# Kernel tuning notes

Measured on AMD Instinct MI355X. Metric: run time of the kernel, lower is better.

Reference implementation:

```python
import jax, jax.numpy as jnp
import numpy as np

HEAD_DIM = 128
PROJ_DIM = 64


def setup_inputs() -> dict:
    key = jax.random.key(0)
    kq, kk, kv, kr = jax.random.split(key, 4)
    B, H, NQ, NKV = 1, 16, 2048, 4096
    Q = jax.random.normal(kq, (B, H, NQ, HEAD_DIM), dtype=jnp.float32)
    K = jax.random.normal(kk, (B, H, NKV, HEAD_DIM), dtype=jnp.float32)
    V = jax.random.normal(kv, (B, H, NKV, HEAD_DIM), dtype=jnp.float32)
    # R ~ N(0,1) / sqrt(proj_dim), as in the torch __init__
    R = jax.random.normal(kr, (HEAD_DIM, PROJ_DIM), dtype=jnp.float32) / (PROJ_DIM ** 0.5)
    return {"Q": Q, "K": K, "V": V, "R": R}


def reference(Q, K, V, R):
    proj_dim = R.shape[-1]
    scale = 1.0 / (proj_dim ** 0.5)
    # Project Q and K into the random-projection space: [B,H,N,proj_dim]
    Q_proj = jnp.einsum('bhnd,dp->bhnp', Q, R)
    K_proj = jnp.einsum('bhmd,dp->bhmp', K, R)
    # scores: [B,H,NQ,NKV]
    scores = jnp.einsum('bhnp,bhmp->bhnm', Q_proj, K_proj) * scale
    weights = jax.nn.softmax(scores, axis=-1)
    # output: [B,H,NQ,head_dim]
    return jnp.einsum('bhnm,bhmd->bhnd', weights, V)
```

## Files before the change

### kernel.cpp

```cpp
#include <hip/hip_runtime.h>

#define HEADS 16
#define NQ    2048
#define NKV   4096
#define DH    128
#define PDIM  64

typedef __bf16 bf16_t;
typedef bf16_t bf16x8 __attribute__((ext_vector_type(8)));
typedef bf16_t bf16x4 __attribute__((ext_vector_type(4)));
typedef bf16_t bf16x2 __attribute__((ext_vector_type(2)));
typedef float  f32x4  __attribute__((ext_vector_type(4)));
typedef float  f32x16 __attribute__((ext_vector_type(16)));
typedef int    i32x4  __attribute__((ext_vector_type(4)));

typedef __attribute__((address_space(3))) unsigned int       lds_u32;
typedef __attribute__((address_space(1))) const unsigned int glb_u32;

__device__ __forceinline__ void dma16(const void* g, void* l) {
  __builtin_amdgcn_global_load_lds((glb_u32*)g, (lds_u32*)l, 16, 0, 0);
}

__global__ __launch_bounds__(256) void rprep_kernel(
    const float* __restrict__ R, bf16_t* __restrict__ Rbt)
{
  const int tid = threadIdx.x;
#pragma unroll
  for (int rep = 0; rep < 32; ++rep) {
    const int idx = tid + rep * 256;
    const int n = idx & 63, k = idx >> 6;
    Rbt[n * 128 + k] = (bf16_t)R[k * 64 + n];
  }
}

__global__ __launch_bounds__(256) void proj_kernel(
    const float* __restrict__ Q, const float* __restrict__ K,
    const bf16_t* __restrict__ Rbt,
    bf16_t* __restrict__ Qp, bf16_t* __restrict__ Kp)
{
  __shared__ bf16_t sY[4][16 * 72];
  const int tid = threadIdx.x;
  const int bid = blockIdx.x;

  const int isQ = (bid < 512);
  const float* src = isQ ? Q : K;
  const long row0  = isQ ? (long)bid * 64 : (long)(bid - 512) * 64;
  const float scale = isQ ? 0.18033688011112042f : 1.0f;
  bf16_t* Y = isQ ? Qp : Kp;

  const int wave = tid >> 6, lane = tid & 63;
  const int n16  = lane & 15, quad = lane >> 4;

  bf16x8 bfr[4][4];
#pragma unroll
  for (int nt = 0; nt < 4; ++nt)
#pragma unroll
    for (int kk = 0; kk < 4; ++kk)
      bfr[nt][kk] = *(const bf16x8*)(Rbt + (nt * 16 + n16) * 128 + kk * 32 + quad * 8);

  const int arow = wave * 16 + n16;
  const float* xp = src + (row0 + arow) * DH;
  bf16x8 a[4];
#pragma unroll
  for (int kk = 0; kk < 4; ++kk) {
    const int k0 = kk * 32 + quad * 8;
    f32x4 x0 = *(const f32x4*)(xp + k0);
    f32x4 x1 = *(const f32x4*)(xp + k0 + 4);
    bf16x8 av;
#pragma unroll
    for (int j = 0; j < 4; ++j) { av[j] = (bf16_t)(x0[j] * scale); av[4 + j] = (bf16_t)(x1[j] * scale); }
    a[kk] = av;
  }

  bf16_t* sy = sY[wave];
#pragma unroll
  for (int nt = 0; nt < 4; ++nt) {
    f32x4 acc = {0.f, 0.f, 0.f, 0.f};
#pragma unroll
    for (int kk = 0; kk < 4; ++kk)
      acc = __builtin_amdgcn_mfma_f32_16x16x32_bf16(a[kk], bfr[nt][kk], acc, 0, 0, 0);
#pragma unroll
    for (int r = 0; r < 4; ++r)
      sy[(quad * 4 + r) * 72 + nt * 16 + n16] = (bf16_t)acc[r];
  }
  const long xrow = row0 + wave * 16;
  const int row = lane >> 2, cg = lane & 3;
  bf16x8 w0 = *(const bf16x8*)(&sy[row * 72 + cg * 16]);
  bf16x8 w1 = *(const bf16x8*)(&sy[row * 72 + cg * 16 + 8]);
  *(bf16x8*)(Y + (xrow + row) * PDIM + cg * 16)     = w0;
  *(bf16x8*)(Y + (xrow + row) * PDIM + cg * 16 + 8) = w1;
}

__global__ __launch_bounds__(256) void vtrans_kernel(
    const float* __restrict__ V, bf16_t* __restrict__ Vt)
{
  __shared__ float sF[64 * 128];
  const int tid = threadIdx.x;
  const int bid = blockIdx.x;

  const float* tp = V + (long)bid * 64 * DH;
#pragma unroll
  for (int rep = 0; rep < 8; ++rep) {
    const int slot = tid + rep * 256;
    const int j = slot >> 5, g = slot & 31;
    f32x4 v = *(const f32x4*)(tp + j * DH + g * 4);
    *(f32x4*)(&sF[j * 128 + ((g ^ ((j >> 3) & 7)) << 2)]) = v;
  }
  __syncthreads();

  const int h = bid >> 6, jt = bid & 63;
  bf16_t* op = Vt + (long)h * DH * NKV + jt * 64;
#pragma unroll
  for (int rep = 0; rep < 4; ++rep) {
    const int slot = tid + rep * 256;
    const int d = slot >> 3, j8 = (slot & 7) * 8;
    const int key = slot & 7;
    const int gsw = (((d >> 2) ^ key) << 2) + (d & 3);
    bf16x8 w;
#pragma unroll
    for (int jj = 0; jj < 8; ++jj) w[jj] = (bf16_t)sF[(j8 + jj) * 128 + gsw];
    *(bf16x8*)(op + (long)d * NKV + j8) = w;
  }
}

__global__ __launch_bounds__(128, 2) void flash_kernel(
    const bf16_t* __restrict__ Qp, const bf16_t* __restrict__ Kp,
    const bf16_t* __restrict__ Vt, bf16_t* __restrict__ Opart,
    float* __restrict__ Lpart, float* __restrict__ Out,
    int splits, int iters)
{
  __shared__ char smem[24576];
  bf16_t* sK = (bf16_t*)smem;
  bf16_t* sV = (bf16_t*)(smem + 8192);

  const int tid  = threadIdx.x;
  const int wave = tid >> 6, lane = tid & 63;
  const int l31  = lane & 31, h = lane >> 5;

  const int head = blockIdx.x & 15;
  const int qt   = (blockIdx.x >> 4) & 15;
  const int sp   = blockIdx.x >> 8;

  const int qbase = qt * 128 + wave * 64;
  const int kv0   = sp * (64 * iters);

  bf16x8 qf[2][4];
#pragma unroll
  for (int qsub = 0; qsub < 2; ++qsub)
#pragma unroll
    for (int k = 0; k < 4; ++k)
      qf[qsub][k] = *(const bf16x8*)(Qp + ((long)head * NQ + qbase + qsub * 32 + l31) * PDIM
                                     + k * 16 + h * 8);

  f32x16 o[2][4] = {};
  float rsum[2] = {0.f, 0.f};

  const bf16_t* kpH = Kp + (long)head * NKV * PDIM;
  const bf16_t* vtH = Vt + (long)head * DH * NKV;

  const int sw = ((lane & 7) ^ ((lane >> 3) & 7)) * 8;
  const int r8 = lane >> 3;

  for (int t = 0; t < iters; ++t) {
    const int kvb = kv0 + t * 64;
    __syncthreads();
    if (wave == 0) {
#pragma unroll
      for (int i = 0; i < 8; ++i)
        dma16(kpH + (long)(kvb + i * 8 + r8) * PDIM + sw, smem + i * 1024);
#pragma unroll
      for (int i = 0; i < 4; ++i)
        dma16(vtH + (long)(i * 8 + r8) * NKV + kvb + sw, smem + 8192 + i * 1024);
    } else {
#pragma unroll
      for (int i = 4; i < 16; ++i)
        dma16(vtH + (long)(i * 8 + r8) * NKV + kvb + sw, smem + 8192 + i * 1024);
    }
    __syncthreads();

#pragma unroll
    for (int s = 0; s < 2; ++s) {
      int bfr[2][2][4];
#pragma unroll
      for (int qsub = 0; qsub < 2; ++qsub) {
        f32x16 sc = {};
        const int r = s * 32 + l31;
#pragma unroll
        for (int k = 0; k < 4; ++k) {
          const int c = 2 * k + h;
          const bf16x8 a = *(const bf16x8*)(sK + r * 64 + ((c ^ (r & 7)) * 8));
          sc = __builtin_amdgcn_mfma_f32_32x32x16_bf16(a, qf[qsub][k], sc, 0, 0, 0);
        }
        int pk[4][2];
#pragma unroll
        for (int rg = 0; rg < 4; ++rg) {
          const float p0 = __builtin_amdgcn_exp2f(sc[rg * 4 + 0]);
          const float p1 = __builtin_amdgcn_exp2f(sc[rg * 4 + 1]);
          const float p2 = __builtin_amdgcn_exp2f(sc[rg * 4 + 2]);
          const float p3 = __builtin_amdgcn_exp2f(sc[rg * 4 + 3]);
          rsum[qsub] += (p0 + p1) + (p2 + p3);
          union { bf16x2 v; int i; } u0, u1;
          u0.v = bf16x2{(bf16_t)p0, (bf16_t)p1};
          u1.v = bf16x2{(bf16_t)p2, (bf16_t)p3};
          pk[rg][0] = u0.i; pk[rg][1] = u1.i;
        }
#pragma unroll
        for (int cl = 0; cl < 2; ++cl) {
          const int e00 = __shfl_xor(pk[2 * cl][0], 32);
          const int e01 = __shfl_xor(pk[2 * cl][1], 32);
          const int e10 = __shfl_xor(pk[2 * cl + 1][0], 32);
          const int e11 = __shfl_xor(pk[2 * cl + 1][1], 32);
          bfr[qsub][cl][0] = h ? e10 : pk[2 * cl][0];
          bfr[qsub][cl][1] = h ? e11 : pk[2 * cl][1];
          bfr[qsub][cl][2] = h ? pk[2 * cl + 1][0] : e00;
          bfr[qsub][cl][3] = h ? pk[2 * cl + 1][1] : e01;
        }
      }
#pragma unroll
      for (int dsub = 0; dsub < 4; ++dsub) {
        const int r = dsub * 32 + l31;
#pragma unroll
        for (int cl = 0; cl < 2; ++cl) {
          const int c = 2 * (2 * s + cl) + h;
          const bf16x8 va = *(const bf16x8*)(sV + r * 64 + ((c ^ (r & 7)) * 8));
#pragma unroll
          for (int qsub = 0; qsub < 2; ++qsub) {
            union { i32x4 i; bf16x8 v; } pb;
            pb.i = i32x4{bfr[qsub][cl][0], bfr[qsub][cl][1],
                         bfr[qsub][cl][2], bfr[qsub][cl][3]};
            o[qsub][dsub] = __builtin_amdgcn_mfma_f32_32x32x16_bf16(va, pb.v, o[qsub][dsub], 0, 0, 0);
          }
        }
      }
    }
  }

  __syncthreads();
  bf16_t* myT = (bf16_t*)(smem + wave * 8704);
#pragma unroll
  for (int qsub = 0; qsub < 2; ++qsub) {
    const float lsum = rsum[qsub] + __shfl_xor(rsum[qsub], 32);
    const float scale = (splits > 1) ? 1.0f : (1.0f / lsum);
#pragma unroll
    for (int dsub = 0; dsub < 4; ++dsub)
#pragma unroll
      for (int rg = 0; rg < 4; ++rg) {
        bf16x4 w = { (bf16_t)(o[qsub][dsub][rg * 4 + 0] * scale),
                     (bf16_t)(o[qsub][dsub][rg * 4 + 1] * scale),
                     (bf16_t)(o[qsub][dsub][rg * 4 + 2] * scale),
                     (bf16_t)(o[qsub][dsub][rg * 4 + 3] * scale) };
        *(bf16x4*)(myT + l31 * 136 + dsub * 32 + rg * 8 + h * 4) = w;
      }
    const int qglob = qbase + qsub * 32;
#pragma unroll
    for (int j = 0; j < 8; ++j) {
      const int ql = j * 4 + (lane >> 4);
      bf16x8 v = *(const bf16x8*)(myT + ql * 136 + (lane & 15) * 8);
      if (splits > 1) {
        *(bf16x8*)(Opart + (((long)sp * HEADS + head) * NQ + qglob + ql) * DH + (lane & 15) * 8) = v;
      } else {
        float* op = Out + ((long)head * NQ + qglob + ql) * DH + (lane & 15) * 8;
        f32x4 a = {(float)v[0], (float)v[1], (float)v[2], (float)v[3]};
        f32x4 b = {(float)v[4], (float)v[5], (float)v[6], (float)v[7]};
        *(f32x4*)op = a; *(f32x4*)(op + 4) = b;
      }
    }
    if (splits > 1 && h == 0)
      Lpart[((long)sp * HEADS + head) * NQ + qglob + l31] = lsum;
  }
}

__global__ __launch_bounds__(256) void combine_kernel(
    const bf16_t* __restrict__ Opart, const float* __restrict__ Lpart,
    float* __restrict__ Out)
{
  const long idx = (long)blockIdx.x * 256 + threadIdx.x;
  const int  d8  = (int)(idx & 15);
  const long hq  = idx >> 4;
  float l = 0.f;
  float acc[8];
#pragma unroll
  for (int j = 0; j < 8; ++j) acc[j] = 0.f;
#pragma unroll
  for (int s = 0; s < 4; ++s) {
    l += Lpart[s * (long)(HEADS * NQ) + hq];
    bf16x8 v = *(const bf16x8*)(Opart + (s * (long)(HEADS * NQ) + hq) * DH + d8 * 8);
#pragma unroll
    for (int j = 0; j < 8; ++j) acc[j] += (float)v[j];
  }
  const float inv = 1.f / l;
  f32x4 o0 = { acc[0] * inv, acc[1] * inv, acc[2] * inv, acc[3] * inv };
  f32x4 o1 = { acc[4] * inv, acc[5] * inv, acc[6] * inv, acc[7] * inv };
  float* op = Out + hq * DH + d8 * 8;
  *(f32x4*)(op)     = o0;
  *(f32x4*)(op + 4) = o1;
}

extern "C" void kernel_launch(void* const* d_in, const int* in_sizes, int n_in,
                              void* d_out, int out_size, void* d_ws, size_t ws_size,
                              hipStream_t stream)
{
  const float* Q = (const float*)d_in[0];
  const float* K = (const float*)d_in[1];
  const float* V = (const float*)d_in[2];
  const float* R = (const float*)d_in[3];
  float* Out = (float*)d_out;

  char* ws = (char*)d_ws;
  bf16_t* Qp = (bf16_t*)(ws);
  bf16_t* Kp = (bf16_t*)(ws + (size_t)(4  << 20));
  bf16_t* Vt = (bf16_t*)(ws + (size_t)(12 << 20));
  bf16_t* Opart = (bf16_t*)(ws + (size_t)(28 << 20));
  float*  Lpart = (float*)(ws + (size_t)(60 << 20));
  bf16_t* Rbt = (bf16_t*)(ws + (size_t)(28 << 20));

  const size_t need4 = (size_t)(60 << 20) + 4ull * HEADS * NQ * sizeof(float);
  const int splits = (ws_size >= need4) ? 4 : 1;
  const int iters  = NKV / (64 * splits);

  rprep_kernel<<<1, 256, 0, stream>>>(R, Rbt);
  proj_kernel<<<1536, 256, 0, stream>>>(Q, K, Rbt, Qp, Kp);
  vtrans_kernel<<<1024, 256, 0, stream>>>(V, Vt);
  flash_kernel<<<splits * 256, 128, 0, stream>>>(Qp, Kp, Vt, Opart, Lpart, Out,
                                                 splits, iters);
  if (splits == 4)
    combine_kernel<<<2048, 256, 0, stream>>>(Opart, Lpart, Out);
}
```

Baseline: 205.2 us.

## Fuse R prep, Q/K projection and V transpose into one prep kernel

Merges three preprocessing kernels into a single launch. Blocks below 1536 do the Q/K projection and blocks from 1536 up do the V transpose. Each projection block now converts R to bf16 and transposes it into padded LDS itself, so the single-block rprep kernel and its workspace buffer are gone. This removes two kernel launches and the serial dependency on the one-block R prep. In exchange, every projection block redoes the R conversion (32 KB of reads per block, mostly hitting cache) and uses 32 KB of LDS, which may lower occupancy.

```diff
diff --git a/kernel.cpp b/kernel.cpp
--- a/kernel.cpp
+++ b/kernel.cpp
@@ -21,26 +21,46 @@
   __builtin_amdgcn_global_load_lds((glb_u32*)g, (lds_u32*)l, 16, 0, 0);
 }
 
-__global__ __launch_bounds__(256) void rprep_kernel(
-    const float* __restrict__ R, bf16_t* __restrict__ Rbt)
+__global__ __launch_bounds__(256) void prep_kernel(
+    const float* __restrict__ Q, const float* __restrict__ K,
+    const float* __restrict__ V, const float* __restrict__ R,
+    bf16_t* __restrict__ Qp, bf16_t* __restrict__ Kp, bf16_t* __restrict__ Vt)
 {
-  const int tid = threadIdx.x;
-#pragma unroll
-  for (int rep = 0; rep < 32; ++rep) {
-    const int idx = tid + rep * 256;
-    const int n = idx & 63, k = idx >> 6;
-    Rbt[n * 128 + k] = (bf16_t)R[k * 64 + n];
-  }
-}
-
-__global__ __launch_bounds__(256) void proj_kernel(
-    const float* __restrict__ Q, const float* __restrict__ K,
-    const bf16_t* __restrict__ Rbt,
-    bf16_t* __restrict__ Qp, bf16_t* __restrict__ Kp)
-{
-  __shared__ bf16_t sY[4][16 * 72];
+  __shared__ char lds[32768];
   const int tid = threadIdx.x;
   const int bid = blockIdx.x;
+
+  if (bid >= 1536) {
+    float* sF = (float*)lds;
+    const int vb = bid - 1536;
+    const float* tp = V + (long)vb * 64 * DH;
+#pragma unroll
+    for (int rep = 0; rep < 8; ++rep) {
+      const int slot = tid + rep * 256;
+      const int j = slot >> 5, g = slot & 31;
+      f32x4 v = *(const f32x4*)(tp + j * DH + g * 4);
+      *(f32x4*)(&sF[j * 128 + ((g ^ ((j >> 3) & 7)) << 2)]) = v;
+    }
+    __syncthreads();
+
+    const int h = vb >> 6, jt = vb & 63;
+    bf16_t* op = Vt + (long)h * DH * NKV + jt * 64;
+#pragma unroll
+    for (int rep = 0; rep < 4; ++rep) {
+      const int slot = tid + rep * 256;
+      const int d = slot >> 3, j8 = (slot & 7) * 8;
+      const int key = slot & 7;
+      const int gsw = (((d >> 2) ^ key) << 2) + (d & 3);
+      bf16x8 w;
+#pragma unroll
+      for (int jj = 0; jj < 8; ++jj) w[jj] = (bf16_t)sF[(j8 + jj) * 128 + gsw];
+      *(bf16x8*)(op + (long)d * NKV + j8) = w;
+    }
+    return;
+  }
+
+  bf16_t* sR = (bf16_t*)lds;
+  bf16_t* sYb = (bf16_t*)(lds + 64 * 136 * 2);
 
   const int isQ = (bid < 512);
   const float* src = isQ ? Q : K;
@@ -48,6 +68,13 @@
   const float scale = isQ ? 0.18033688011112042f : 1.0f;
   bf16_t* Y = isQ ? Qp : Kp;
 
+#pragma unroll
+  for (int rep = 0; rep < 32; ++rep) {
+    const int idx = tid + rep * 256;
+    sR[(idx & 63) * 136 + (idx >> 6)] = (bf16_t)R[idx];
+  }
+  __syncthreads();
+
   const int wave = tid >> 6, lane = tid & 63;
   const int n16  = lane & 15, quad = lane >> 4;
 
@@ -56,7 +83,7 @@
   for (int nt = 0; nt < 4; ++nt)
 #pragma unroll
     for (int kk = 0; kk < 4; ++kk)
-      bfr[nt][kk] = *(const bf16x8*)(Rbt + (nt * 16 + n16) * 128 + kk * 32 + quad * 8);
+      bfr[nt][kk] = *(const bf16x8*)(sR + (nt * 16 + n16) * 136 + kk * 32 + quad * 8);
 
   const int arow = wave * 16 + n16;
   const float* xp = src + (row0 + arow) * DH;
@@ -72,7 +99,7 @@
     a[kk] = av;
   }
 
-  bf16_t* sy = sY[wave];
+  bf16_t* sy = sYb + wave * (16 * 72);
 #pragma unroll
   for (int nt = 0; nt < 4; ++nt) {
     f32x4 acc = {0.f, 0.f, 0.f, 0.f};
@@ -89,38 +116,6 @@
   bf16x8 w1 = *(const bf16x8*)(&sy[row * 72 + cg * 16 + 8]);
   *(bf16x8*)(Y + (xrow + row) * PDIM + cg * 16)     = w0;
   *(bf16x8*)(Y + (xrow + row) * PDIM + cg * 16 + 8) = w1;
-}
-
-__global__ __launch_bounds__(256) void vtrans_kernel(
-    const float* __restrict__ V, bf16_t* __restrict__ Vt)
-{
-  __shared__ float sF[64 * 128];
-  const int tid = threadIdx.x;
-  const int bid = blockIdx.x;
-
-  const float* tp = V + (long)bid * 64 * DH;
-#pragma unroll
-  for (int rep = 0; rep < 8; ++rep) {
-    const int slot = tid + rep * 256;
-    const int j = slot >> 5, g = slot & 31;
-    f32x4 v = *(const f32x4*)(tp + j * DH + g * 4);
-    *(f32x4*)(&sF[j * 128 + ((g ^ ((j >> 3) & 7)) << 2)]) = v;
-  }
-  __syncthreads();
-
-  const int h = bid >> 6, jt = bid & 63;
-  bf16_t* op = Vt + (long)h * DH * NKV + jt * 64;
-#pragma unroll
-  for (int rep = 0; rep < 4; ++rep) {
-    const int slot = tid + rep * 256;
-    const int d = slot >> 3, j8 = (slot & 7) * 8;
-    const int key = slot & 7;
-    const int gsw = (((d >> 2) ^ key) << 2) + (d & 3);
-    bf16x8 w;
-#pragma unroll
-    for (int jj = 0; jj < 8; ++jj) w[jj] = (bf16_t)sF[(j8 + jj) * 128 + gsw];
-    *(bf16x8*)(op + (long)d * NKV + j8) = w;
-  }
 }
 
 __global__ __launch_bounds__(128, 2) void flash_kernel(
@@ -312,15 +307,12 @@
   bf16_t* Vt = (bf16_t*)(ws + (size_t)(12 << 20));
   bf16_t* Opart = (bf16_t*)(ws + (size_t)(28 << 20));
   float*  Lpart = (float*)(ws + (size_t)(60 << 20));
-  bf16_t* Rbt = (bf16_t*)(ws + (size_t)(28 << 20));
 
   const size_t need4 = (size_t)(60 << 20) + 4ull * HEADS * NQ * sizeof(float);
   const int splits = (ws_size >= need4) ? 4 : 1;
   const int iters  = NKV / (64 * splits);
 
-  rprep_kernel<<<1, 256, 0, stream>>>(R, Rbt);
-  proj_kernel<<<1536, 256, 0, stream>>>(Q, K, Rbt, Qp, Kp);
-  vtrans_kernel<<<1024, 256, 0, stream>>>(V, Vt);
+  prep_kernel<<<2560, 256, 0, stream>>>(Q, K, V, R, Qp, Kp, Vt);
   flash_kernel<<<splits * 256, 128, 0, stream>>>(Qp, Kp, Vt, Opart, Lpart, Out,
                                                  splits, iters);
   if (splits == 4)
```

Result: faster. 194.1 us (-5.4%).
